# Performance work log

Measured on AMD Instinct MI355X. Metric: run time of the kernel, lower is better.

Reference implementation:

```python
import jax, jax.numpy as jnp
import numpy as np
import itertools

GRID = 256          # voxel grid extent per axis (coords in [0, GRID))
KSIZE = 3           # kernel_size
OFFSETS = np.array(list(itertools.product(range(KSIZE), repeat=3)), dtype=np.int32) - (KSIZE // 2)  # [27,3]


def setup_inputs() -> dict:
    key = jax.random.key(0)
    k1, k2, k3 = jax.random.split(key, 3)
    N, Cin, Cout = 262144, 64, 64
    coords = jax.random.randint(k1, (N, 3), 0, GRID, dtype=jnp.int32)
    feats = jax.random.normal(k2, (N, Cin), dtype=jnp.float32)
    kernel = jax.random.normal(k3, (KSIZE ** 3, Cin, Cout), dtype=jnp.float32) * 0.02
    return {"coords": coords, "feats": feats, "kernel": kernel}


def reference(coords, feats, kernel):
    # Submanifold sparse conv3d: out[i] = sum_k feats[j_k(i)] @ kernel[k]
    # where coords[j_k(i)] == coords[i] + offset_k (if such a point exists).
    N = coords.shape[0]
    Cout = kernel.shape[-1]
    # Hash table: linearized voxel -> point index (-1 if empty).
    lin = (coords[:, 0] * GRID + coords[:, 1]) * GRID + coords[:, 2]
    table = jnp.full((GRID ** 3,), -1, dtype=jnp.int32).at[lin].set(
        jnp.arange(N, dtype=jnp.int32))
    out = jnp.zeros((N, Cout), dtype=feats.dtype)
    for k in range(KSIZE ** 3):
        off = jnp.asarray(OFFSETS[k])              # [3]
        nc = coords + off[None, :]                 # neighbor coords [N,3]
        in_bounds = jnp.all((nc >= 0) & (nc < GRID), axis=1)
        nlin = (nc[:, 0] * GRID + nc[:, 1]) * GRID + nc[:, 2]
        idx = table[jnp.clip(nlin, 0, GRID ** 3 - 1)]
        valid = in_bounds & (idx >= 0)
        g = feats[jnp.where(valid, idx, 0)] * valid[:, None].astype(feats.dtype)  # [N,Cin]
        out = out + g @ kernel[k]                  # [N,Cout]
    return out
```

## Files before the change

kernel.cpp:

```cpp
#include <hip/hip_runtime.h>

#define VGRID 256
#define N_TAPS 27
#define CIN 64
#define COUT 64
#define BPTS 128
#define HBITS 20
#define HSIZE (1u << HBITS)
#define HEMPTY 0xFFFFFFFFFFFFFFFFull

typedef short short8 __attribute__((ext_vector_type(8)));
typedef float float4v __attribute__((ext_vector_type(4)));

__device__ __forceinline__ short f2bf(float x) {
    unsigned u = __builtin_bit_cast(unsigned, x);
    unsigned r = (u + 0x7FFF + ((u >> 16) & 1)) >> 16;
    return (short)r;
}

__device__ __forceinline__ unsigned hslot(int lin) {
    return ((unsigned)lin * 2654435761u) >> (32 - HBITS);
}

__device__ __forceinline__ int hlookup(const unsigned long long* __restrict__ hash,
                                       int lin) {
    unsigned s = hslot(lin);
    for (;;) {
        unsigned long long e = hash[s];
        if ((unsigned)(e >> 32) == (unsigned)lin) return (int)(unsigned)e;
        s = (s + 1) & (HSIZE - 1);
    }
}

__global__ void __launch_bounds__(256) build_kernel(
        const int* __restrict__ coords, unsigned long long* __restrict__ hash,
        unsigned* __restrict__ bits, const float* __restrict__ W,
        short* __restrict__ Wt, const float* __restrict__ F,
        short* __restrict__ Fb, int n, int bt_blocks, int fb_elems) {
    int b = (int)blockIdx.x;
    if (b >= bt_blocks + N_TAPS) {
        int idx = (b - bt_blocks - N_TAPS) * 256 + (int)threadIdx.x;
        int e = idx * 8;
        if (e < fb_elems) {
            const float4v* s = (const float4v*)(F + e);
            float4v x = __builtin_nontemporal_load(s);
            float4v y = __builtin_nontemporal_load(s + 1);
            short8 o = {f2bf(x[0]), f2bf(x[1]), f2bf(x[2]), f2bf(x[3]),
                        f2bf(y[0]), f2bf(y[1]), f2bf(y[2]), f2bf(y[3])};
            *(short8*)(Fb + e) = o;
        }
        return;
    }
    if (b >= bt_blocks) {
        int tap = b - bt_blocks;
        for (int e = threadIdx.x; e < CIN * COUT; e += 256) {
            int ci = e >> 6, co = e & 63;
            int ks = ci >> 5, quad = (ci >> 3) & 3, el = ci & 7;
            Wt[((((size_t)tap * 2 + ks) * 4 + quad) * 64 + co) * 8 + el] =
                f2bf(W[((size_t)tap * CIN + ci) * COUT + co]);
        }
        return;
    }
    int i = b * 256 + threadIdx.x;
    if (i >= n) return;
    int lin = (coords[i * 3 + 0] * VGRID + coords[i * 3 + 1]) * VGRID + coords[i * 3 + 2];
    unsigned long long want = ((unsigned long long)(unsigned)lin << 32) | (unsigned)i;
    unsigned s = hslot(lin);
    for (;;) {
        unsigned long long old = atomicCAS(&hash[s], HEMPTY, want);
        if (old == HEMPTY) break;
        if ((unsigned)(old >> 32) == (unsigned)lin) { atomicMax(&hash[s], want); break; }
        s = (s + 1) & (HSIZE - 1);
    }
    atomicOr(&bits[lin >> 5], 1u << (lin & 31));
}

__global__ void __launch_bounds__(256) fused_kernel(
        const int* __restrict__ coords, const unsigned long long* __restrict__ hash,
        const unsigned* __restrict__ bits, const short* __restrict__ featsb,
        const short* __restrict__ Wt, float* __restrict__ out, int n) {
    __shared__ int s_pk[BPTS];
    __shared__ unsigned s_hm[2][BPTS];
    __shared__ int s_jc[BPTS];
    __shared__ int s_p[4][BPTS];

    int t = threadIdx.x;
    int p = t & (BPTS - 1);
    int h = t >> 7;
    int i = blockIdx.x * BPTS + p;

    int cx = 0, cy = 0, cz = 0;
    unsigned pmask = 0;
    if (i < n) {
        cx = coords[i * 3 + 0];
        cy = coords[i * 3 + 1];
        cz = coords[i * 3 + 2];
        if (h == 0) s_jc[p] = hlookup(hash, (cx * VGRID + cy) * VGRID + cz);

        int zlo = cz > 0 ? cz - 1 : 0;
        int zhi = cz < VGRID - 1 ? cz + 1 : VGRID - 1;
        int wlo = zlo >> 5, whi = zhi >> 5;
        unsigned rwa[5], rwb[5];
#pragma unroll
        for (int rr = 0; rr < 5; ++rr) {
            int r = h * 5 + rr;
            int nx = cx + r / 3 - 1, ny = cy + r % 3 - 1;
            bool v = (r < 9) && ((unsigned)nx < VGRID) && ((unsigned)ny < VGRID);
            int rb = ((nx * VGRID + ny) * VGRID) >> 5;
            rwa[rr] = v ? bits[rb + wlo] : 0u;
            rwb[rr] = v ? bits[rb + whi] : 0u;
        }
#pragma unroll
        for (int rr = 0; rr < 5; ++rr) {
            int r = h * 5 + rr;
#pragma unroll
            for (int zz = 0; zz < 3; ++zz) {
                int k = r * 3 + zz;
                int nz = cz + zz - 1;
                if (r < 9 && k != 13 && (unsigned)nz < VGRID) {
                    unsigned wrd = ((nz >> 5) == wlo) ? rwa[rr] : rwb[rr];
                    pmask |= ((wrd >> (nz & 31)) & 1u) << k;
                }
            }
        }
    }
    if (h == 0) {
        s_pk[p] = (cx << 16) | (cy << 8) | cz;
        if (i >= n) s_jc[p] = 0;
    }
    s_hm[h][p] = pmask;
    __syncthreads();

    {
        unsigned hmc = s_hm[0][p] | s_hm[1][p];
        if (h == 0) s_hm[0][p] = hmc;
        unsigned mm = hmc;
        if (h) { mm &= mm - 1u; if (mm) mm &= mm - 1u; }
        int kA = -1, kB = -1;
        if (mm) { kA = __builtin_ctz(mm); mm &= mm - 1u;
                  if (mm) kB = __builtin_ctz(mm); }
        int ja = 0, jb = 0;
        if (kA >= 0)
            ja = hlookup(hash, ((cx + kA / 9 - 1) * VGRID + (cy + (kA / 3) % 3 - 1)) * VGRID
                               + (cz + kA % 3 - 1));
        if (kB >= 0)
            jb = hlookup(hash, ((cx + kB / 9 - 1) * VGRID + (cy + (kB / 3) % 3 - 1)) * VGRID
                               + (cz + kB % 3 - 1));
        s_p[2 * h + 0][p] = ja;
        s_p[2 * h + 1][p] = jb;
    }
    __syncthreads();

    int wave = t >> 6, lane = t & 63;
    int m = lane & 15, quad = lane >> 4;
    const short8* Bp = (const short8*)Wt;
    const short8* Fp = (const short8*)featsb;
    int base = blockIdx.x * BPTS;

    for (int gg = 0; gg < 2; ++gg) {
        int g = wave * 2 + gg;
        int row = g * 16 + m;
        unsigned rhm = s_hm[0][row];
        int rjc = s_jc[row];

        unsigned gor = rhm;
        gor |= (unsigned)__shfl_xor((int)gor, 1);
        gor |= (unsigned)__shfl_xor((int)gor, 2);
        gor |= (unsigned)__shfl_xor((int)gor, 4);
        gor |= (unsigned)__shfl_xor((int)gor, 8);
        gor = __builtin_amdgcn_readfirstlane(gor);

        float4v acc[4] = {{0,0,0,0},{0,0,0,0},{0,0,0,0},{0,0,0,0}};

        auto loadfrag = [&](int k, short8& f0, short8& f1) {
            int j2 = -1;
            if (k == 13) {
                j2 = rjc;
            } else if ((rhm >> k) & 1u) {
                int rank = __builtin_popcount(rhm & ((1u << k) - 1u));
                if (rank < 4) {
                    j2 = s_p[rank][row];
                } else {
                    int rpk = s_pk[row];
                    int rx = (rpk >> 16) & 255, ry = (rpk >> 8) & 255, rz = rpk & 255;
                    j2 = hlookup(hash, ((rx + k / 9 - 1) * VGRID + (ry + (k / 3) % 3 - 1))
                                       * VGRID + (rz + k % 3 - 1));
                }
            }
            f0 = (short8){0,0,0,0,0,0,0,0};
            f1 = (short8){0,0,0,0,0,0,0,0};
            if (j2 >= 0) {
                f0 = Fp[(size_t)j2 * 8 + quad];
                f1 = Fp[(size_t)j2 * 8 + 4 + quad];
            }
        };

        unsigned gm = gor | (1u << 13);
        while (gm) {
            int k0 = (int)__builtin_ctz(gm); gm &= gm - 1u;
            int k1 = -1;
            if (gm) { k1 = (int)__builtin_ctz(gm); gm &= gm - 1u; }

            short8 x0, x1, y0, y1;
            loadfrag(k0, x0, x1);
            if (k1 >= 0) loadfrag(k1, y0, y1);

#pragma unroll
            for (int nt = 0; nt < 4; ++nt) {
                short8 b0 = Bp[((k0 * 2 + 0) * 4 + quad) * 64 + nt * 16 + m];
                short8 b1 = Bp[((k0 * 2 + 1) * 4 + quad) * 64 + nt * 16 + m];
                acc[nt] = __builtin_amdgcn_mfma_f32_16x16x32_bf16(x0, b0, acc[nt], 0, 0, 0);
                acc[nt] = __builtin_amdgcn_mfma_f32_16x16x32_bf16(x1, b1, acc[nt], 0, 0, 0);
            }
            if (k1 >= 0) {
#pragma unroll
                for (int nt = 0; nt < 4; ++nt) {
                    short8 b0 = Bp[((k1 * 2 + 0) * 4 + quad) * 64 + nt * 16 + m];
                    short8 b1 = Bp[((k1 * 2 + 1) * 4 + quad) * 64 + nt * 16 + m];
                    acc[nt] = __builtin_amdgcn_mfma_f32_16x16x32_bf16(y0, b0, acc[nt], 0, 0, 0);
                    acc[nt] = __builtin_amdgcn_mfma_f32_16x16x32_bf16(y1, b1, acc[nt], 0, 0, 0);
                }
            }
        }

#pragma unroll
        for (int nt = 0; nt < 4; ++nt)
#pragma unroll
            for (int r2 = 0; r2 < 4; ++r2) {
                int orow = base + g * 16 + quad * 4 + r2;
                if (orow < n)
                    __builtin_nontemporal_store(
                        acc[nt][r2], &out[(size_t)orow * COUT + nt * 16 + m]);
            }
    }
}

extern "C" void kernel_launch(void* const* d_in, const int* in_sizes, int n_in,
                              void* d_out, int out_size, void* d_ws, size_t ws_size,
                              hipStream_t stream) {
    const int* coords = (const int*)d_in[0];
    const float* feats = (const float*)d_in[1];
    const float* weights = (const float*)d_in[2];
    float* out = (float*)d_out;

    int n = in_sizes[0] / 3;

    char* ws = (char*)d_ws;
    size_t BITMAP_BYTES = (size_t)VGRID * VGRID * VGRID / 8;
    unsigned* bits = (unsigned*)ws;
    unsigned long long* hash = (unsigned long long*)(ws + BITMAP_BYTES);
    short* wbft = (short*)(ws + ((size_t)10 << 20));
    short* fb = (short*)(ws + ((size_t)11 << 20));

    hipMemsetAsync(ws, 0, BITMAP_BYTES, stream);
    hipMemsetAsync(ws + BITMAP_BYTES, 0xFF, (size_t)HSIZE * 8, stream);

    int bt_blocks = (n + 255) / 256;
    int fb_elems = n * CIN;
    int conv_blocks = (fb_elems / 8 + 255) / 256;
    build_kernel<<<bt_blocks + N_TAPS + conv_blocks, 256, 0, stream>>>(
        coords, hash, bits, weights, wbft, feats, fb, n, bt_blocks, fb_elems);

    int f_blocks = (n + BPTS - 1) / BPTS;
    fused_kernel<<<f_blocks, 256, 0, stream>>>(coords, hash, bits, fb, wbft, out, n);
}
```

Baseline: 211.0 us.

## Shrink block to 64 points with four threads per point and one row group per wave

Halves points per block and splits the neighbor bitmap scan and first-neighbor hash lookups across four threads per point instead of two. Each wave now handles a single 16-row group, not two, which doubles the grid size for more parallelism and latency hiding. The center tap is processed unconditionally up front, and the main loop handles one tap per iteration instead of two. The output store switches from nontemporal to a regular store, and losing the two-tap unroll may reduce memory-level parallelism per wave.

After: 207.4 us. About the same (-1.7%).

```diff
diff --git a/kernel.cpp b/kernel.cpp
--- a/kernel.cpp
+++ b/kernel.cpp
@@ -4,7 +4,7 @@
 #define N_TAPS 27
 #define CIN 64
 #define COUT 64
-#define BPTS 128
+#define BPTS 64
 #define HBITS 20
 #define HSIZE (1u << HBITS)
 #define HEMPTY 0xFFFFFFFFFFFFFFFFull
@@ -80,13 +80,13 @@
         const unsigned* __restrict__ bits, const short* __restrict__ featsb,
         const short* __restrict__ Wt, float* __restrict__ out, int n) {
     __shared__ int s_pk[BPTS];
-    __shared__ unsigned s_hm[2][BPTS];
+    __shared__ unsigned s_hm[4][BPTS];
     __shared__ int s_jc[BPTS];
     __shared__ int s_p[4][BPTS];
 
     int t = threadIdx.x;
     int p = t & (BPTS - 1);
-    int h = t >> 7;
+    int q = t >> 6;
     int i = blockIdx.x * BPTS + p;
 
     int cx = 0, cy = 0, cz = 0;
@@ -95,144 +95,126 @@
         cx = coords[i * 3 + 0];
         cy = coords[i * 3 + 1];
         cz = coords[i * 3 + 2];
-        if (h == 0) s_jc[p] = hlookup(hash, (cx * VGRID + cy) * VGRID + cz);
+        if (q == 0) s_jc[p] = hlookup(hash, (cx * VGRID + cy) * VGRID + cz);
 
         int zlo = cz > 0 ? cz - 1 : 0;
         int zhi = cz < VGRID - 1 ? cz + 1 : VGRID - 1;
         int wlo = zlo >> 5, whi = zhi >> 5;
-        unsigned rwa[5], rwb[5];
-#pragma unroll
-        for (int rr = 0; rr < 5; ++rr) {
-            int r = h * 5 + rr;
+        int nr = (q == 3) ? 3 : 2;
+        int r0 = 2 * q;
+        unsigned rwa[3], rwb[3];
+#pragma unroll
+        for (int rr = 0; rr < 3; ++rr) {
+            int r = r0 + rr;
             int nx = cx + r / 3 - 1, ny = cy + r % 3 - 1;
-            bool v = (r < 9) && ((unsigned)nx < VGRID) && ((unsigned)ny < VGRID);
+            bool v = (rr < nr) && ((unsigned)nx < VGRID) && ((unsigned)ny < VGRID);
             int rb = ((nx * VGRID + ny) * VGRID) >> 5;
             rwa[rr] = v ? bits[rb + wlo] : 0u;
             rwb[rr] = v ? bits[rb + whi] : 0u;
         }
 #pragma unroll
-        for (int rr = 0; rr < 5; ++rr) {
-            int r = h * 5 + rr;
+        for (int rr = 0; rr < 3; ++rr) {
+            int r = r0 + rr;
 #pragma unroll
             for (int zz = 0; zz < 3; ++zz) {
                 int k = r * 3 + zz;
                 int nz = cz + zz - 1;
-                if (r < 9 && k != 13 && (unsigned)nz < VGRID) {
+                if (rr < nr && k != 13 && (unsigned)nz < VGRID) {
                     unsigned wrd = ((nz >> 5) == wlo) ? rwa[rr] : rwb[rr];
                     pmask |= ((wrd >> (nz & 31)) & 1u) << k;
                 }
             }
         }
     }
-    if (h == 0) {
+    if (q == 0) {
         s_pk[p] = (cx << 16) | (cy << 8) | cz;
         if (i >= n) s_jc[p] = 0;
     }
-    s_hm[h][p] = pmask;
+    s_hm[q][p] = pmask;
     __syncthreads();
 
     {
-        unsigned hmc = s_hm[0][p] | s_hm[1][p];
-        if (h == 0) s_hm[0][p] = hmc;
+        unsigned hmc = s_hm[0][p] | s_hm[1][p] | s_hm[2][p] | s_hm[3][p];
+        if (q == 0) s_hm[0][p] = hmc;
         unsigned mm = hmc;
-        if (h) { mm &= mm - 1u; if (mm) mm &= mm - 1u; }
-        int kA = -1, kB = -1;
-        if (mm) { kA = __builtin_ctz(mm); mm &= mm - 1u;
-                  if (mm) kB = __builtin_ctz(mm); }
-        int ja = 0, jb = 0;
-        if (kA >= 0)
-            ja = hlookup(hash, ((cx + kA / 9 - 1) * VGRID + (cy + (kA / 3) % 3 - 1)) * VGRID
-                               + (cz + kA % 3 - 1));
-        if (kB >= 0)
-            jb = hlookup(hash, ((cx + kB / 9 - 1) * VGRID + (cy + (kB / 3) % 3 - 1)) * VGRID
-                               + (cz + kB % 3 - 1));
-        s_p[2 * h + 0][p] = ja;
-        s_p[2 * h + 1][p] = jb;
+#pragma unroll
+        for (int d = 0; d < 3; ++d) if (d < q) mm &= mm - 1u;
+        int ja = 0;
+        if (mm) {
+            int kA = __builtin_ctz(mm);
+            ja = hlookup(hash, ((cx + kA / 9 - 1) * VGRID + (cy + (kA / 3) % 3 - 1))
+                               * VGRID + (cz + kA % 3 - 1));
+        }
+        s_p[q][p] = ja;
     }
     __syncthreads();
 
-    int wave = t >> 6, lane = t & 63;
+    int lane = t & 63;
     int m = lane & 15, quad = lane >> 4;
     const short8* Bp = (const short8*)Wt;
     const short8* Fp = (const short8*)featsb;
     int base = blockIdx.x * BPTS;
 
-    for (int gg = 0; gg < 2; ++gg) {
-        int g = wave * 2 + gg;
-        int row = g * 16 + m;
-        unsigned rhm = s_hm[0][row];
-        int rjc = s_jc[row];
-
-        unsigned gor = rhm;
-        gor |= (unsigned)__shfl_xor((int)gor, 1);
-        gor |= (unsigned)__shfl_xor((int)gor, 2);
-        gor |= (unsigned)__shfl_xor((int)gor, 4);
-        gor |= (unsigned)__shfl_xor((int)gor, 8);
-        gor = __builtin_amdgcn_readfirstlane(gor);
-
-        float4v acc[4] = {{0,0,0,0},{0,0,0,0},{0,0,0,0},{0,0,0,0}};
-
-        auto loadfrag = [&](int k, short8& f0, short8& f1) {
-            int j2 = -1;
-            if (k == 13) {
-                j2 = rjc;
-            } else if ((rhm >> k) & 1u) {
-                int rank = __builtin_popcount(rhm & ((1u << k) - 1u));
-                if (rank < 4) {
-                    j2 = s_p[rank][row];
-                } else {
-                    int rpk = s_pk[row];
-                    int rx = (rpk >> 16) & 255, ry = (rpk >> 8) & 255, rz = rpk & 255;
-                    j2 = hlookup(hash, ((rx + k / 9 - 1) * VGRID + (ry + (k / 3) % 3 - 1))
-                                       * VGRID + (rz + k % 3 - 1));
-                }
+    int row = q * 16 + m;
+    unsigned rhm = s_hm[0][row];
+    int rjc = s_jc[row];
+
+    unsigned gor = rhm;
+    gor |= (unsigned)__shfl_xor((int)gor, 1);
+    gor |= (unsigned)__shfl_xor((int)gor, 2);
+    gor |= (unsigned)__shfl_xor((int)gor, 4);
+    gor |= (unsigned)__shfl_xor((int)gor, 8);
+    gor = __builtin_amdgcn_readfirstlane(gor);
+
+    float4v acc[4] = {{0,0,0,0},{0,0,0,0},{0,0,0,0},{0,0,0,0}};
+
+    {
+        short8 a0 = Fp[(size_t)rjc * 8 + quad];
+        short8 a1 = Fp[(size_t)rjc * 8 + 4 + quad];
+#pragma unroll
+        for (int nt = 0; nt < 4; ++nt) {
+            short8 b0 = Bp[((13 * 2 + 0) * 4 + quad) * 64 + nt * 16 + m];
+            short8 b1 = Bp[((13 * 2 + 1) * 4 + quad) * 64 + nt * 16 + m];
+            acc[nt] = __builtin_amdgcn_mfma_f32_16x16x32_bf16(a0, b0, acc[nt], 0, 0, 0);
+            acc[nt] = __builtin_amdgcn_mfma_f32_16x16x32_bf16(a1, b1, acc[nt], 0, 0, 0);
+        }
+    }
+
+    unsigned gm = gor;
+    while (gm) {
+        int k = (int)__builtin_ctz(gm); gm &= gm - 1u;
+        bool has = (rhm >> k) & 1u;
+        short8 h0 = {0,0,0,0,0,0,0,0}, h1 = {0,0,0,0,0,0,0,0};
+        if (has) {
+            int rank = __builtin_popcount(rhm & ((1u << k) - 1u));
+            int j2;
+            if (rank < 4) {
+                j2 = s_p[rank][row];
+            } else {
+                int rpk = s_pk[row];
+                int rx = (rpk >> 16) & 255, ry = (rpk >> 8) & 255, rz = rpk & 255;
+                j2 = hlookup(hash, ((rx + k / 9 - 1) * VGRID + (ry + (k / 3) % 3 - 1))
+                                   * VGRID + (rz + k % 3 - 1));
             }
-            f0 = (short8){0,0,0,0,0,0,0,0};
-            f1 = (short8){0,0,0,0,0,0,0,0};
-            if (j2 >= 0) {
-                f0 = Fp[(size_t)j2 * 8 + quad];
-                f1 = Fp[(size_t)j2 * 8 + 4 + quad];
-            }
-        };
-
-        unsigned gm = gor | (1u << 13);
-        while (gm) {
-            int k0 = (int)__builtin_ctz(gm); gm &= gm - 1u;
-            int k1 = -1;
-            if (gm) { k1 = (int)__builtin_ctz(gm); gm &= gm - 1u; }
-
-            short8 x0, x1, y0, y1;
-            loadfrag(k0, x0, x1);
-            if (k1 >= 0) loadfrag(k1, y0, y1);
-
-#pragma unroll
-            for (int nt = 0; nt < 4; ++nt) {
-                short8 b0 = Bp[((k0 * 2 + 0) * 4 + quad) * 64 + nt * 16 + m];
-                short8 b1 = Bp[((k0 * 2 + 1) * 4 + quad) * 64 + nt * 16 + m];
-                acc[nt] = __builtin_amdgcn_mfma_f32_16x16x32_bf16(x0, b0, acc[nt], 0, 0, 0);
-                acc[nt] = __builtin_amdgcn_mfma_f32_16x16x32_bf16(x1, b1, acc[nt], 0, 0, 0);
-            }
-            if (k1 >= 0) {
-#pragma unroll
-                for (int nt = 0; nt < 4; ++nt) {
-                    short8 b0 = Bp[((k1 * 2 + 0) * 4 + quad) * 64 + nt * 16 + m];
-                    short8 b1 = Bp[((k1 * 2 + 1) * 4 + quad) * 64 + nt * 16 + m];
-                    acc[nt] = __builtin_amdgcn_mfma_f32_16x16x32_bf16(y0, b0, acc[nt], 0, 0, 0);
-                    acc[nt] = __builtin_amdgcn_mfma_f32_16x16x32_bf16(y1, b1, acc[nt], 0, 0, 0);
-                }
-            }
-        }
-
-#pragma unroll
-        for (int nt = 0; nt < 4; ++nt)
-#pragma unroll
-            for (int r2 = 0; r2 < 4; ++r2) {
-                int orow = base + g * 16 + quad * 4 + r2;
-                if (orow < n)
-                    __builtin_nontemporal_store(
-                        acc[nt][r2], &out[(size_t)orow * COUT + nt * 16 + m]);
-            }
-    }
+            h0 = Fp[(size_t)j2 * 8 + quad];
+            h1 = Fp[(size_t)j2 * 8 + 4 + quad];
+        }
+#pragma unroll
+        for (int nt = 0; nt < 4; ++nt) {
+            short8 b0 = Bp[((k * 2 + 0) * 4 + quad) * 64 + nt * 16 + m];
+            short8 b1 = Bp[((k * 2 + 1) * 4 + quad) * 64 + nt * 16 + m];
+            acc[nt] = __builtin_amdgcn_mfma_f32_16x16x32_bf16(h0, b0, acc[nt], 0, 0, 0);
+            acc[nt] = __builtin_amdgcn_mfma_f32_16x16x32_bf16(h1, b1, acc[nt], 0, 0, 0);
+        }
+    }
+
+#pragma unroll
+    for (int nt = 0; nt < 4; ++nt)
+#pragma unroll
+        for (int r2 = 0; r2 < 4; ++r2) {
+            int orow = base + q * 16 + quad * 4 + r2;
+            if (orow < n) out[(size_t)orow * COUT + nt * 16 + m] = acc[nt][r2];
+        }
 }
 
 extern "C" void kernel_launch(void* const* d_in, const int* in_sizes, int n_in,
```
